# Kernel optimization log

Hardware: AMD Instinct MI355X
Metric: run time of the kernel (lower is better)

The kernel has to match this reference:

```python
import jax, jax.numpy as jnp
import numpy as np

NUM_SITES = 64
BOND_DIM = 64
PHYS_DIM = 2
BATCH = 8192
INIT_STD = 0.125  # 1/sqrt(bond_dim)
EPS_AMP = 1e-12
EPS_LOG = 1e-30


def setup_inputs() -> dict:
    key = jax.random.key(0)
    k_cfg, k_l, k_b, k_r = jax.random.split(key, 4)
    configurations = jax.random.randint(k_cfg, (BATCH, NUM_SITES), 0, PHYS_DIM, dtype=jnp.int32)
    left = jax.random.normal(k_l, (PHYS_DIM, BOND_DIM), dtype=jnp.float32) * INIT_STD
    bulk = jax.random.normal(k_b, (NUM_SITES - 2, BOND_DIM, PHYS_DIM, BOND_DIM), dtype=jnp.float32) * INIT_STD
    right = jax.random.normal(k_r, (BOND_DIM, PHYS_DIM), dtype=jnp.float32) * INIT_STD
    return {"configurations": configurations, "left": left, "bulk": bulk, "right": right}


def _psi(configurations, left, bulk, right):
    # configurations: [B, S] int; left: [d, D]; bulk: [S-2, D, d, D]; right: [D, d]
    B = configurations.shape[0]
    env0 = left[configurations[:, 0]]  # [B, D]
    cfg_mid = configurations[:, 1:-1].T  # [S-2, B]

    def step(env, xs):
        site_t, idx = xs  # site_t: [D, d, D], idx: [B]
        D = site_t.shape[0]
        # env @ site (contract left bond), then gather the per-sample physical slice
        tmp = (env @ site_t.reshape(D, -1)).reshape(B, PHYS_DIM, D)  # [B, d, D]
        env = jnp.take_along_axis(tmp, idx[:, None, None], axis=1)[:, 0, :]  # [B, D]
        return env, None

    env, _ = jax.lax.scan(step, env0, (bulk, cfg_mid))
    cols = jnp.take(right, configurations[:, -1], axis=1).T  # [B, D]
    return jnp.sum(env * cols, axis=1)  # [B]


def _log_norm(left, bulk, right):
    env0 = left.T @ left  # [D, D]  (real dtype -> conj trivial)

    def step(carry, site_t):
        env, log_scale = carry
        sm = jnp.transpose(site_t, (1, 0, 2))  # [d, D, D]
        env = jnp.einsum('pdi,de,pej->ij', sm, env, sm)  # sum_p A_p^H env A_p
        scale = jnp.maximum(jnp.max(jnp.abs(env)), EPS_LOG)
        return (env / scale, log_scale + jnp.log(scale)), None

    (env, log_scale), _ = jax.lax.scan(step, (env0, jnp.zeros((), left.dtype)), bulk)
    z = jnp.sum(right * (env @ right))
    return jnp.log(jnp.maximum(z, EPS_LOG)) + log_scale


def reference(configurations, left, bulk, right):
    psi = _psi(configurations, left, bulk, right)
    abs_sq = jnp.maximum(psi * psi, EPS_AMP)
    log_z = _log_norm(left, bulk, right)
    nll = -(jnp.log(abs_sq) - log_z)
    return jnp.mean(nll)
```

## Files before the change

kernel.cpp:

```cpp
#include <hip/hip_runtime.h>
#include <math.h>

#define NBULK 62
#define SB    72

typedef __attribute__((ext_vector_type(8))) short bf8_t;
typedef __attribute__((ext_vector_type(4))) float f4_t;
typedef __attribute__((ext_vector_type(16))) float f16v_t;

#define MFMA16(a, b, c) __builtin_amdgcn_mfma_f32_16x16x32_bf16((a), (b), (c), 0, 0, 0)
#define MFMA32(a, b, c) __builtin_amdgcn_mfma_f32_32x32x16_bf16((a), (b), (c), 0, 0, 0)

__device__ __forceinline__ unsigned short f2bf(float f) {
    unsigned int u = __float_as_uint(f);
    return (unsigned short)((u + 0x7FFFu + ((u >> 16) & 1u)) >> 16);
}
__device__ __forceinline__ float bf2f(unsigned short h) {
    return __uint_as_float(((unsigned int)h) << 16);
}
__device__ __forceinline__ unsigned cvtpk(float lo, float hi) {
    unsigned r;
    asm("v_cvt_pk_bf16_f32 %0, %1, %2" : "=v"(r) : "v"(lo), "v"(hi));
    return r;
}

__device__ __forceinline__ void gload16(const void* g, void* l) {
    __builtin_amdgcn_global_load_lds(
        (const __attribute__((address_space(1))) unsigned int*)g,
        (__attribute__((address_space(3))) unsigned int*)l, 16, 0, 0);
}

#define WS_E_OFF   1024
#define WS_B_OFF   6144
#define WS_BT_OFF  45056
#define WS_MR_OFF  1060864


extern "C" __global__ __launch_bounds__(256)
void mps_precompute(const float* __restrict__ bulkG,
                    unsigned short* __restrict__ BTg,
                    unsigned short* __restrict__ MRg,
                    float* __restrict__ wsF)
{
    __shared__ unsigned short BTl[8192];
    __shared__ unsigned short MRl[8192];
    const int s = blockIdx.x, tid = threadIdx.x;
    if (s == 0 && tid == 0) {
        wsF[0] = 0.f; wsF[1] = 0.f; wsF[2] = 0.f; wsF[3] = 0.f;
    }
    const float4* src = (const float4*)(bulkG + (size_t)s * 8192);
    for (int c = 0; c < 8; ++c) {
        int idx = tid + c * 256;
        float4 v = src[idx];
        int f  = idx * 4;
        int kk = f >> 7;
        int p  = (f >> 6) & 1;
        int j  = f & 63;
        unsigned short b0 = f2bf(v.x), b1 = f2bf(v.y), b2 = f2bf(v.z), b3 = f2bf(v.w);
        int n = p * 64 + kk;
        int off = n * 64 + (((j >> 3) ^ (n & 7)) << 3) + (j & 7);
        MRl[off + 0] = b0; MRl[off + 1] = b1; MRl[off + 2] = b2; MRl[off + 3] = b3;
        unsigned short bb[4] = {b0, b1, b2, b3};
        #pragma unroll
        for (int t2 = 0; t2 < 4; ++t2) {
            int n2 = p * 64 + j + t2;
            BTl[n2 * 64 + (((kk >> 3) ^ (n2 & 7)) << 3) + (kk & 7)] = bb[t2];
        }
    }
    __syncthreads();
    const uint4* bt4 = (const uint4*)BTl;
    const uint4* mr4 = (const uint4*)MRl;
    uint4* btg = (uint4*)(BTg + (size_t)s * 8192);
    uint4* mrg = (uint4*)(MRg + (size_t)s * 8192);
    for (int c = 0; c < 4; ++c) {
        int idx = tid + c * 256;
        btg[idx] = bt4[idx];
        mrg[idx] = mr4[idx];
    }
}

__device__ __forceinline__ void psi_phase(
    uint4 (&R)[16], int tt, unsigned short* env, const char* BTb,
    const int (&off)[4], unsigned selLo, unsigned selHi,
    int s, int hi, int e7, const f16v_t& Z)
{
    bf8_t benv[4];
    #pragma unroll
    for (int ks = 0; ks < 4; ++ks)
        benv[ks] = *(const bf8_t*)((const char*)env + s * 128 + (((ks * 2 + hi) ^ e7) << 4));
    unsigned sbit = (tt + 1 < 32) ? (selLo >> (tt + 1)) : (selHi >> (tt - 31));
    const bool takeB = (sbit & 1u) != 0u;
    #pragma unroll
    for (int jt = 0; jt < 2; ++jt) {
        f16v_t a0 = Z, a1 = Z;
        #pragma unroll
        for (int ks = 0; ks < 4; ++ks) {
            a0 = MFMA32(*(const bf8_t*)&R[jt * 4 + ks],     benv[ks], a0);
            a1 = MFMA32(*(const bf8_t*)&R[8 + jt * 4 + ks], benv[ks], a1);
        }
        #pragma unroll
        for (int b = 0; b < 4; ++b) {
            float v0 = takeB ? a1[4 * b + 0] : a0[4 * b + 0];
            float v1 = takeB ? a1[4 * b + 1] : a0[4 * b + 1];
            float v2 = takeB ? a1[4 * b + 2] : a0[4 * b + 2];
            float v3 = takeB ? a1[4 * b + 3] : a0[4 * b + 3];
            uint2 w;
            w.x = cvtpk(v0, v1);
            w.y = cvtpk(v2, v3);
            *(uint2*)((char*)env + s * 128 + (((jt * 4 + b) ^ e7) << 4) + hi * 8) = w;
        }
    }
    if (tt + 2 < NBULK) {
        const char* tb = BTb + (size_t)(tt + 2) * 16384;
        #pragma unroll
        for (int p = 0; p < 2; ++p)
            #pragma unroll
            for (int jt = 0; jt < 2; ++jt)
                #pragma unroll
                for (int ks = 0; ks < 4; ++ks)
                    R[p * 8 + jt * 4 + ks] =
                        *(const uint4*)(tb + p * 8192 + jt * 4096 + off[ks]);
    }
}

extern "C" __global__ __launch_bounds__(256)
void mps_main(const int* __restrict__ cfgG, const float* __restrict__ leftG,
              const float* __restrict__ rightG, float* __restrict__ wsF,
              const unsigned short* __restrict__ BTg,
              const unsigned short* __restrict__ MRg)
{
    extern __shared__ char smem[];
    unsigned short* smem16 = (unsigned short*)smem;
    const int tid  = threadIdx.x;
    const int bid  = blockIdx.x;
    const int wv   = tid >> 6;
    const int lane = tid & 63;

    if (bid >= 2) {
        if (wv >= 2) return;
        const int s  = lane & 31;
        const int hi = lane >> 5;
        const int e7 = lane & 7;
        unsigned short* env = smem16 + wv * 2048;
        const int s0 = (bid - 2) * 64 + wv * 32;

        int off[4];
        #pragma unroll
        for (int ks = 0; ks < 4; ++ks)
            off[ks] = s * 128 + (((ks * 2 + hi) ^ e7) << 4);

        const char* BTb = (const char*)BTg;
        uint4 ra[16], rb[16];
        #pragma unroll
        for (int p = 0; p < 2; ++p)
            #pragma unroll
            for (int jt = 0; jt < 2; ++jt)
                #pragma unroll
                for (int ks = 0; ks < 4; ++ks) {
                    ra[p * 8 + jt * 4 + ks] = *(const uint4*)(BTb + p * 8192 + jt * 4096 + off[ks]);
                    rb[p * 8 + jt * 4 + ks] = *(const uint4*)(BTb + 16384 + p * 8192 + jt * 4096 + off[ks]);
                }

        unsigned mbits = 0;
        {
            const int4* crow = (const int4*)(cfgG + (size_t)(s0 + s) * 64 + hi * 32);
            #pragma unroll
            for (int c = 0; c < 8; ++c) {
                int4 v = crow[c];
                mbits |= (unsigned)(v.x & 1) << (c * 4 + 0);
                mbits |= (unsigned)(v.y & 1) << (c * 4 + 1);
                mbits |= (unsigned)(v.z & 1) << (c * 4 + 2);
                mbits |= (unsigned)(v.w & 1) << (c * 4 + 3);
            }
        }
        unsigned other = __shfl_xor(mbits, 32);
        unsigned selLo = hi ? other : mbits;
        unsigned selHi = hi ? mbits : other;

        {
            const float* lp = leftG + (selLo & 1u) * 64 + hi * 32;
            #pragma unroll
            for (int gg = 0; gg < 4; ++gg) {
                float4 a = *(const float4*)(lp + gg * 8);
                float4 b = *(const float4*)(lp + gg * 8 + 4);
                uint4 w;
                w.x = (unsigned)f2bf(a.x) | ((unsigned)f2bf(a.y) << 16);
                w.y = (unsigned)f2bf(a.z) | ((unsigned)f2bf(a.w) << 16);
                w.z = (unsigned)f2bf(b.x) | ((unsigned)f2bf(b.y) << 16);
                w.w = (unsigned)f2bf(b.z) | ((unsigned)f2bf(b.w) << 16);
                int g = hi * 4 + gg;
                *(uint4*)((char*)env + s * 128 + ((g ^ e7) << 4)) = w;
            }
        }

        const f16v_t Z = {0.f};
        for (int t = 0; t < NBULK; t += 2) {
            psi_phase(ra, t,     env, BTb, off, selLo, selHi, s, hi, e7, Z);
            psi_phase(rb, t + 1, env, BTb, off, selLo, selHi, s, hi, e7, Z);
        }

        {
            int selL = (selHi >> 31) & 1;
            float psum = 0.f;
            #pragma unroll
            for (int gg = 0; gg < 4; ++gg) {
                int g = hi * 4 + gg;
                bf8_t e = *(const bf8_t*)((const char*)env + s * 128 + ((g ^ e7) << 4));
                #pragma unroll
                for (int j = 0; j < 8; ++j)
                    psum = fmaf(bf2f((unsigned short)e[j]), rightG[(g * 8 + j) * 2 + selL], psum);
            }
            psum += __shfl_xor(psum, 32);
            float lp = logf(fmaxf(psum * psum, 1e-12f));
            if (hi) lp = 0.f;
            #pragma unroll
            for (int o = 1; o < 64; o <<= 1) lp += __shfl_xor(lp, o);
            if (lane == 0) atomicAdd(&wsF[0], lp);
        }
    } else {
        unsigned short* Ebf = smem16;
        unsigned short* St0 = Ebf + 64 * SB;
        unsigned short* St1 = St0 + 64 * SB;
        unsigned short* Ms0 = St1 + 64 * SB;
        unsigned short* Ms1 = Ms0 + 8192;
        float* wred = (float*)(Ms1 + 8192);

        const int quad = lane >> 4;
        const int ln   = lane & 15;
        const bool fwd = (bid == 0);
        const unsigned short* srcbase = fwd ? BTg : MRg;
        {
            int i = tid >> 2, jq = tid & 3;
            for (int jj = 0; jj < 16; ++jj) {
                int j = jq * 16 + jj;
                float v;
                if (fwd) v = leftG[i] * leftG[j] + leftG[64 + i] * leftG[64 + j];
                else     v = rightG[i * 2] * rightG[j * 2] + rightG[i * 2 + 1] * rightG[j * 2 + 1];
                Ebf[i * SB + j] = f2bf(v);
            }
        }
        {
            int st = fwd ? 0 : 61;
            const char* g = (const char*)(srcbase + (size_t)st * 8192);
            for (int c = 0; c < 4; ++c) {
                int chunk = wv * 4 + c;
                gload16(g + chunk * 1024 + (size_t)lane * 16, (char*)Ms0 + chunk * 1024);
            }
        }
        float lsum = 0.f;
        const int p   = wv >> 1;
        const int ntb = (wv & 1) * 2;
        const int mta = (wv >> 1) * 2;
        const int nta = (wv & 1) * 2;
        unsigned short* Stp = p ? St1 : St0;

        for (int k = 0; k < 31; ++k) {
            __syncthreads();
            unsigned short* M = (k & 1) ? Ms1 : Ms0;
            if (k + 1 < 31) {
                int sn = fwd ? (k + 1) : (61 - (k + 1));
                const char* g = (const char*)(srcbase + (size_t)sn * 8192);
                char* l = (char*)((k & 1) ? Ms0 : Ms1);
                for (int c = 0; c < 4; ++c) {
                    int chunk = wv * 4 + c;
                    gload16(g + chunk * 1024 + (size_t)lane * 16, l + chunk * 1024);
                }
            }
            float inv = 1.f;
            if (k > 0) {
                const float* wp = wred + ((k - 1) & 1) * 4;
                float mm = fmaxf(fmaxf(wp[0], wp[1]), fmaxf(wp[2], wp[3]));
                float sc = fmaxf(mm, 1e-30f);
                inv = 1.f / sc;
                if (tid == 0) lsum += logf(sc);
            }
            {
                bf8_t Af2[4][2];
                #pragma unroll
                for (int mt = 0; mt < 4; ++mt)
                    #pragma unroll
                    for (int h = 0; h < 2; ++h)
                        Af2[mt][h] = *(const bf8_t*)(Ebf + (mt * 16 + ln) * SB + h * 32 + quad * 8);
                #pragma unroll
                for (int c = 0; c < 2; ++c) {
                    int nt = ntb + c;
                    int row = p * 64 + nt * 16 + ln;
                    bf8_t B0 = *(const bf8_t*)(M + row * 64 + (((0 + quad) ^ (ln & 7)) << 3));
                    bf8_t B1 = *(const bf8_t*)(M + row * 64 + (((4 + quad) ^ (ln & 7)) << 3));
                    #pragma unroll
                    for (int mt = 0; mt < 4; ++mt) {
                        f4_t a = {0.f, 0.f, 0.f, 0.f};
                        a = MFMA16(Af2[mt][0], B0, a);
                        a = MFMA16(Af2[mt][1], B1, a);
                        ushort4 pk;
                        pk.x = f2bf(a[0]); pk.y = f2bf(a[1]); pk.z = f2bf(a[2]); pk.w = f2bf(a[3]);
                        *(ushort4*)(Stp + (nt * 16 + ln) * SB + mt * 16 + quad * 4) = pk;
                    }
                }
            }
            asm volatile("s_waitcnt lgkmcnt(0)" ::: "memory");
            __builtin_amdgcn_s_barrier();
            __builtin_amdgcn_sched_barrier(0);
            {
                bf8_t Aw[2][2][2], Bw[2][2][2];
                #pragma unroll
                for (int pp = 0; pp < 2; ++pp)
                    #pragma unroll
                    for (int mi = 0; mi < 2; ++mi)
                        #pragma unroll
                        for (int h = 0; h < 2; ++h)
                            Aw[pp][mi][h] = *(const bf8_t*)(M + (pp * 64 + (mta + mi) * 16 + ln) * 64
                                                              + (((h * 4 + quad) ^ (ln & 7)) << 3));
                #pragma unroll
                for (int pp = 0; pp < 2; ++pp)
                    #pragma unroll
                    for (int ni = 0; ni < 2; ++ni)
                        #pragma unroll
                        for (int h = 0; h < 2; ++h)
                            Bw[pp][ni][h] = *(const bf8_t*)((pp ? St1 : St0)
                                                            + ((nta + ni) * 16 + ln) * SB + h * 32 + quad * 8);
                float mx = 0.f;
                #pragma unroll
                for (int mi = 0; mi < 2; ++mi)
                    #pragma unroll
                    for (int ni = 0; ni < 2; ++ni) {
                        f4_t a = {0.f, 0.f, 0.f, 0.f};
                        #pragma unroll
                        for (int pp = 0; pp < 2; ++pp)
                            #pragma unroll
                            for (int h = 0; h < 2; ++h)
                                a = MFMA16(Aw[pp][mi][h], Bw[pp][ni][h], a);
                        float x0 = a[0] * inv, x1 = a[1] * inv, x2 = a[2] * inv, x3 = a[3] * inv;
                        mx = fmaxf(mx, fmaxf(fmaxf(fabsf(x0), fabsf(x1)), fmaxf(fabsf(x2), fabsf(x3))));
                        ushort4 pk;
                        pk.x = f2bf(x0); pk.y = f2bf(x1); pk.z = f2bf(x2); pk.w = f2bf(x3);
                        *(ushort4*)(Ebf + ((nta + ni) * 16 + ln) * SB + (mta + mi) * 16 + quad * 4) = pk;
                    }
                #pragma unroll
                for (int off2 = 32; off2 > 0; off2 >>= 1)
                    mx = fmaxf(mx, __shfl_xor(mx, off2));
                if (lane == 0) wred[(k & 1) * 4 + wv] = mx;
            }
        }
        __syncthreads();
        float* dst = wsF + (fwd ? WS_E_OFF : WS_B_OFF);
        for (int c = 0; c < 16; ++c) {
            int idx = tid + c * 256;
            dst[idx] = bf2f(Ebf[(idx >> 6) * SB + (idx & 63)]);
        }
        if (tid == 0) wsF[fwd ? 1 : 2] = lsum;
    }
}

extern "C" __global__ void mps_finalize(const float* __restrict__ wsF, float* __restrict__ out)
{
    const int lane = threadIdx.x;
    const float* E  = wsF + WS_E_OFF;
    const float* Bm = wsF + WS_B_OFF;
    float a = 0.f;
    #pragma unroll 8
    for (int j = 0; j < 64; ++j)
        a = fmaf(E[lane * 64 + j], Bm[lane * 64 + j], a);
    #pragma unroll
    for (int off = 32; off > 0; off >>= 1)
        a += __shfl_down(a, off);
    if (lane == 0) {
        const float z = fmaxf(a, 1e-30f);
        const float log_z = logf(z) + wsF[1] + wsF[2];
        out[0] = log_z - wsF[0] * (1.0f / 8192.0f);
    }
}

extern "C" void kernel_launch(void* const* d_in, const int* in_sizes, int n_in,
                              void* d_out, int out_size, void* d_ws, size_t ws_size,
                              hipStream_t stream)
{
    const int*   cfg   = (const int*)d_in[0];
    const float* left  = (const float*)d_in[1];
    const float* bulk  = (const float*)d_in[2];
    const float* right = (const float*)d_in[3];
    float* wsF = (float*)d_ws;
    unsigned short* BTg = (unsigned short*)((char*)d_ws + WS_BT_OFF);
    unsigned short* MRg = (unsigned short*)((char*)d_ws + WS_MR_OFF);

    mps_precompute<<<dim3(62), dim3(256), 0, stream>>>(bulk, BTg, MRg, wsF);
    mps_main<<<dim3(130), dim3(256), 60480, stream>>>(cfg, left, right, wsF, BTg, MRg);
    mps_finalize<<<dim3(1), dim3(64), 0, stream>>>(wsF, (float*)d_out);
}
```

Before: 119.0 us.

## Keep psi env in registers, use all four waves, fuse finalize into main kernel

The psi chain now passes the environment between sites directly in registers, repacking MFMA accumulators into B operands, so the per-site LDS round trip is gone. All four waves per block now run the chain, so the grid shrinks from 130 to 66 blocks. The separate finalize kernel is replaced by a last-block-done atomic counter inside the main kernel, which saves one launch. In exchange it adds fence and atomic overhead, depends on the counter at wsF[3] being zeroed, and may change the register permutation of env elements.

```diff
diff --git a/kernel.cpp b/kernel.cpp
--- a/kernel.cpp
+++ b/kernel.cpp
@@ -79,144 +79,161 @@
     }
 }
 
-__device__ __forceinline__ void psi_phase(
-    uint4 (&R)[16], int tt, unsigned short* env, const char* BTb,
-    const int (&off)[4], unsigned selLo, unsigned selHi,
-    int s, int hi, int e7, const f16v_t& Z)
-{
-    bf8_t benv[4];
+
+__device__ __forceinline__ void psi_fetch(uint4 (&A)[16], const char* tb,
+                                          const unsigned (&voff)[8])
+{
+    #pragma unroll
+    for (int p = 0; p < 2; ++p)
+        #pragma unroll
+        for (int jt = 0; jt < 2; ++jt) {
+            const char* bb = tb + p * 8192 + jt * 4096;
+            #pragma unroll
+            for (int ks = 0; ks < 4; ++ks) {
+                uint2 lo  = *(const uint2*)(bb + voff[2 * ks]);
+                uint2 hi8 = *(const uint2*)(bb + voff[2 * ks + 1]);
+                uint4& F = A[p * 8 + jt * 4 + ks];
+                F.x = lo.x; F.y = lo.y; F.z = hi8.x; F.w = hi8.y;
+            }
+        }
+}
+
+__device__ __forceinline__ void psi_mfma(f16v_t (&c)[2][2], const uint4 (&A)[16],
+                                         const bf8_t (&B)[4], const f16v_t& Z)
+{
+    #pragma unroll
+    for (int p = 0; p < 2; ++p)
+        #pragma unroll
+        for (int jt = 0; jt < 2; ++jt)
+            c[p][jt] = Z;
     #pragma unroll
     for (int ks = 0; ks < 4; ++ks)
-        benv[ks] = *(const bf8_t*)((const char*)env + s * 128 + (((ks * 2 + hi) ^ e7) << 4));
-    unsigned sbit = (tt + 1 < 32) ? (selLo >> (tt + 1)) : (selHi >> (tt - 31));
-    const bool takeB = (sbit & 1u) != 0u;
-    #pragma unroll
-    for (int jt = 0; jt < 2; ++jt) {
-        f16v_t a0 = Z, a1 = Z;
-        #pragma unroll
-        for (int ks = 0; ks < 4; ++ks) {
-            a0 = MFMA32(*(const bf8_t*)&R[jt * 4 + ks],     benv[ks], a0);
-            a1 = MFMA32(*(const bf8_t*)&R[8 + jt * 4 + ks], benv[ks], a1);
-        }
-        #pragma unroll
-        for (int b = 0; b < 4; ++b) {
-            float v0 = takeB ? a1[4 * b + 0] : a0[4 * b + 0];
-            float v1 = takeB ? a1[4 * b + 1] : a0[4 * b + 1];
-            float v2 = takeB ? a1[4 * b + 2] : a0[4 * b + 2];
-            float v3 = takeB ? a1[4 * b + 3] : a0[4 * b + 3];
-            uint2 w;
-            w.x = cvtpk(v0, v1);
-            w.y = cvtpk(v2, v3);
-            *(uint2*)((char*)env + s * 128 + (((jt * 4 + b) ^ e7) << 4) + hi * 8) = w;
-        }
-    }
-    if (tt + 2 < NBULK) {
-        const char* tb = BTb + (size_t)(tt + 2) * 16384;
         #pragma unroll
         for (int p = 0; p < 2; ++p)
             #pragma unroll
             for (int jt = 0; jt < 2; ++jt)
-                #pragma unroll
-                for (int ks = 0; ks < 4; ++ks)
-                    R[p * 8 + jt * 4 + ks] =
-                        *(const uint4*)(tb + p * 8192 + jt * 4096 + off[ks]);
-    }
-}
-
-extern "C" __global__ __launch_bounds__(256)
+                c[p][jt] = MFMA32(*(const bf8_t*)&A[p * 8 + jt * 4 + ks], B[ks], c[p][jt]);
+}
+
+__device__ __forceinline__ void psi_pack(bf8_t (&B)[4], const f16v_t (&c)[2][2], bool takeB)
+{
+    #pragma unroll
+    for (int ks = 0; ks < 4; ++ks) {
+        const int jt = ks >> 1, h8 = (ks & 1) * 8;
+        uint4 w;
+        float x0, x1;
+        x0 = takeB ? c[1][jt][h8 + 0] : c[0][jt][h8 + 0];
+        x1 = takeB ? c[1][jt][h8 + 1] : c[0][jt][h8 + 1];
+        w.x = cvtpk(x0, x1);
+        x0 = takeB ? c[1][jt][h8 + 2] : c[0][jt][h8 + 2];
+        x1 = takeB ? c[1][jt][h8 + 3] : c[0][jt][h8 + 3];
+        w.y = cvtpk(x0, x1);
+        x0 = takeB ? c[1][jt][h8 + 4] : c[0][jt][h8 + 4];
+        x1 = takeB ? c[1][jt][h8 + 5] : c[0][jt][h8 + 5];
+        w.z = cvtpk(x0, x1);
+        x0 = takeB ? c[1][jt][h8 + 6] : c[0][jt][h8 + 6];
+        x1 = takeB ? c[1][jt][h8 + 7] : c[0][jt][h8 + 7];
+        w.w = cvtpk(x0, x1);
+        B[ks] = *(const bf8_t*)&w;
+    }
+}
+
+extern "C" __global__ __launch_bounds__(256, 1)
 void mps_main(const int* __restrict__ cfgG, const float* __restrict__ leftG,
               const float* __restrict__ rightG, float* __restrict__ wsF,
               const unsigned short* __restrict__ BTg,
-              const unsigned short* __restrict__ MRg)
+              const unsigned short* __restrict__ MRg,
+              float* __restrict__ outG)
 {
     extern __shared__ char smem[];
     unsigned short* smem16 = (unsigned short*)smem;
+    __shared__ int lastf;
     const int tid  = threadIdx.x;
     const int bid  = blockIdx.x;
     const int wv   = tid >> 6;
     const int lane = tid & 63;
 
     if (bid >= 2) {
-        if (wv >= 2) return;
         const int s  = lane & 31;
         const int hi = lane >> 5;
-        const int e7 = lane & 7;
-        unsigned short* env = smem16 + wv * 2048;
-        const int s0 = (bid - 2) * 64 + wv * 32;
-
-        int off[4];
+        unsigned voff[8];
         #pragma unroll
-        for (int ks = 0; ks < 4; ++ks)
-            off[ks] = s * 128 + (((ks * 2 + hi) ^ e7) << 4);
-
+        for (int g = 0; g < 8; ++g)
+            voff[g] = (unsigned)(s * 128 + (((g ^ (s & 7)) << 4) + hi * 8));
         const char* BTb = (const char*)BTg;
-        uint4 ra[16], rb[16];
-        #pragma unroll
-        for (int p = 0; p < 2; ++p)
-            #pragma unroll
-            for (int jt = 0; jt < 2; ++jt)
-                #pragma unroll
-                for (int ks = 0; ks < 4; ++ks) {
-                    ra[p * 8 + jt * 4 + ks] = *(const uint4*)(BTb + p * 8192 + jt * 4096 + off[ks]);
-                    rb[p * 8 + jt * 4 + ks] = *(const uint4*)(BTb + 16384 + p * 8192 + jt * 4096 + off[ks]);
-                }
-
+
+        uint4 Aa[16], Ab[16];
+        psi_fetch(Aa, BTb, voff);
+        psi_fetch(Ab, BTb + 16384, voff);
+
+        const int s0 = (bid - 2) * 128 + wv * 32;
         unsigned mbits = 0;
         {
             const int4* crow = (const int4*)(cfgG + (size_t)(s0 + s) * 64 + hi * 32);
             #pragma unroll
-            for (int c = 0; c < 8; ++c) {
-                int4 v = crow[c];
-                mbits |= (unsigned)(v.x & 1) << (c * 4 + 0);
-                mbits |= (unsigned)(v.y & 1) << (c * 4 + 1);
-                mbits |= (unsigned)(v.z & 1) << (c * 4 + 2);
-                mbits |= (unsigned)(v.w & 1) << (c * 4 + 3);
+            for (int c2 = 0; c2 < 8; ++c2) {
+                int4 v = crow[c2];
+                mbits |= (unsigned)(v.x & 1) << (c2 * 4 + 0);
+                mbits |= (unsigned)(v.y & 1) << (c2 * 4 + 1);
+                mbits |= (unsigned)(v.z & 1) << (c2 * 4 + 2);
+                mbits |= (unsigned)(v.w & 1) << (c2 * 4 + 3);
             }
         }
         unsigned other = __shfl_xor(mbits, 32);
         unsigned selLo = hi ? other : mbits;
         unsigned selHi = hi ? mbits : other;
 
+        bf8_t B[4];
         {
-            const float* lp = leftG + (selLo & 1u) * 64 + hi * 32;
-            #pragma unroll
-            for (int gg = 0; gg < 4; ++gg) {
-                float4 a = *(const float4*)(lp + gg * 8);
-                float4 b = *(const float4*)(lp + gg * 8 + 4);
+            const float* lp = leftG + (selLo & 1u) * 64;
+            #pragma unroll
+            for (int ks = 0; ks < 4; ++ks) {
                 uint4 w;
-                w.x = (unsigned)f2bf(a.x) | ((unsigned)f2bf(a.y) << 16);
-                w.y = (unsigned)f2bf(a.z) | ((unsigned)f2bf(a.w) << 16);
-                w.z = (unsigned)f2bf(b.x) | ((unsigned)f2bf(b.y) << 16);
-                w.w = (unsigned)f2bf(b.z) | ((unsigned)f2bf(b.w) << 16);
-                int g = hi * 4 + gg;
-                *(uint4*)((char*)env + s * 128 + ((g ^ e7) << 4)) = w;
+                unsigned wd[4];
+                #pragma unroll
+                for (int d = 0; d < 4; ++d) {
+                    int k0 = 16 * ks + 8 * (d >> 1) + 2 * (d & 1) + 4 * hi;
+                    wd[d] = (unsigned)f2bf(lp[k0]) | ((unsigned)f2bf(lp[k0 + 1]) << 16);
+                }
+                w.x = wd[0]; w.y = wd[1]; w.z = wd[2]; w.w = wd[3];
+                B[ks] = *(const bf8_t*)&w;
             }
         }
 
         const f16v_t Z = {0.f};
-        for (int t = 0; t < NBULK; t += 2) {
-            psi_phase(ra, t,     env, BTb, off, selLo, selHi, s, hi, e7, Z);
-            psi_phase(rb, t + 1, env, BTb, off, selLo, selHi, s, hi, e7, Z);
-        }
-
+        f16v_t c[2][2];
+        #define SELBIT(i) ((bool)((((i) < 32) ? (selLo >> (i)) : (selHi >> ((i) - 32))) & 1u))
+        for (int t = 0; t < 60; t += 2) {
+            psi_mfma(c, Aa, B, Z);
+            psi_fetch(Aa, BTb + (size_t)(t + 2) * 16384, voff);
+            psi_pack(B, c, SELBIT(t + 1));
+            psi_mfma(c, Ab, B, Z);
+            psi_fetch(Ab, BTb + (size_t)(t + 3) * 16384, voff);
+            psi_pack(B, c, SELBIT(t + 2));
+        }
+        psi_mfma(c, Aa, B, Z);
+        psi_pack(B, c, SELBIT(61));
+        psi_mfma(c, Ab, B, Z);
         {
-            int selL = (selHi >> 31) & 1;
+            const bool tb2 = SELBIT(62);
+            const int selL = (int)(selHi >> 31) & 1;
             float psum = 0.f;
             #pragma unroll
-            for (int gg = 0; gg < 4; ++gg) {
-                int g = hi * 4 + gg;
-                bf8_t e = *(const bf8_t*)((const char*)env + s * 128 + ((g ^ e7) << 4));
-                #pragma unroll
-                for (int j = 0; j < 8; ++j)
-                    psum = fmaf(bf2f((unsigned short)e[j]), rightG[(g * 8 + j) * 2 + selL], psum);
-            }
+            for (int jt = 0; jt < 2; ++jt)
+                #pragma unroll
+                for (int q = 0; q < 16; ++q) {
+                    float v = tb2 ? c[1][jt][q] : c[0][jt][q];
+                    int idx = 32 * jt + (q & 3) + 8 * (q >> 2) + 4 * hi;
+                    psum = fmaf(v, rightG[idx * 2 + selL], psum);
+                }
             psum += __shfl_xor(psum, 32);
-            float lp = logf(fmaxf(psum * psum, 1e-12f));
-            if (hi) lp = 0.f;
-            #pragma unroll
-            for (int o = 1; o < 64; o <<= 1) lp += __shfl_xor(lp, o);
-            if (lane == 0) atomicAdd(&wsF[0], lp);
-        }
+            float lp2 = logf(fmaxf(psum * psum, 1e-12f));
+            if (hi) lp2 = 0.f;
+            #pragma unroll
+            for (int o = 1; o < 64; o <<= 1) lp2 += __shfl_xor(lp2, o);
+            if (lane == 0) atomicAdd(&wsF[0], lp2);
+        }
+        #undef SELBIT
     } else {
         unsigned short* Ebf = smem16;
         unsigned short* St0 = Ebf + 64 * SB;
@@ -298,9 +315,7 @@
                     }
                 }
             }
-            asm volatile("s_waitcnt lgkmcnt(0)" ::: "memory");
-            __builtin_amdgcn_s_barrier();
-            __builtin_amdgcn_sched_barrier(0);
+            __syncthreads();
             {
                 bf8_t Aw[2][2][2], Bw[2][2][2];
                 #pragma unroll
@@ -350,24 +365,29 @@
         }
         if (tid == 0) wsF[fwd ? 1 : 2] = lsum;
     }
-}
-
-extern "C" __global__ void mps_finalize(const float* __restrict__ wsF, float* __restrict__ out)
-{
-    const int lane = threadIdx.x;
-    const float* E  = wsF + WS_E_OFF;
-    const float* Bm = wsF + WS_B_OFF;
-    float a = 0.f;
-    #pragma unroll 8
-    for (int j = 0; j < 64; ++j)
-        a = fmaf(E[lane * 64 + j], Bm[lane * 64 + j], a);
-    #pragma unroll
-    for (int off = 32; off > 0; off >>= 1)
-        a += __shfl_down(a, off);
-    if (lane == 0) {
-        const float z = fmaxf(a, 1e-30f);
-        const float log_z = logf(z) + wsF[1] + wsF[2];
-        out[0] = log_z - wsF[0] * (1.0f / 8192.0f);
+
+    __threadfence();
+    if (tid == 0)
+        lastf = (atomicAdd((int*)&wsF[3], 1) == (int)gridDim.x - 1);
+    __syncthreads();
+    if (lastf) {
+        __threadfence();
+        if (wv == 0) {
+            const float* E  = wsF + WS_E_OFF;
+            const float* Bm = wsF + WS_B_OFF;
+            float a = 0.f;
+            #pragma unroll 8
+            for (int c2 = 0; c2 < 64; ++c2)
+                a = fmaf(E[c2 * 64 + lane], Bm[c2 * 64 + lane], a);
+            #pragma unroll
+            for (int o = 32; o > 0; o >>= 1)
+                a += __shfl_down(a, o);
+            if (lane == 0) {
+                const float z = fmaxf(a, 1e-30f);
+                const float log_z = logf(z) + wsF[1] + wsF[2];
+                outG[0] = log_z - wsF[0] * (1.0f / 8192.0f);
+            }
+        }
     }
 }
 
@@ -384,6 +404,6 @@
     unsigned short* MRg = (unsigned short*)((char*)d_ws + WS_MR_OFF);
 
     mps_precompute<<<dim3(62), dim3(256), 0, stream>>>(bulk, BTg, MRg, wsF);
-    mps_main<<<dim3(130), dim3(256), 60480, stream>>>(cfg, left, right, wsF, BTg, MRg);
-    mps_finalize<<<dim3(1), dim3(64), 0, stream>>>(wsF, (float*)d_out);
-}
+    mps_main<<<dim3(66), dim3(256), 60480, stream>>>(cfg, left, right, wsF, BTg, MRg,
+                                                     (float*)d_out);
+}
```

Result: slower. 214.2 us (+80.1%).

## Keep MPS environments in registers using fragment-native weight layout and 16x16 MFMA

Applied to the files above, without the earlier changes.

The precompute pass now stores each bulk site in an MFMA-fragment-native layout, so each lane fetches its operands with contiguous 16-byte loads. The psi chain keeps its environment in registers: the 16x16x32 MFMA output is repacked straight into the next B operand instead of going through shared memory. All four waves are used with 16 samples each rather than two waves with 32. The norm chain computes each wave's column slice using register-held operands and only exchanges results through a small LDS buffer. This removes LDS round-trips and the dynamic shared allocation, at the cost of more register pressure (launch bounds set to one block) and more global weight traffic per wave.

```diff
diff --git a/kernel.cpp b/kernel.cpp
--- a/kernel.cpp
+++ b/kernel.cpp
@@ -1,15 +1,10 @@
 #include <hip/hip_runtime.h>
 #include <math.h>
 
-#define NBULK 62
-#define SB    72
-
 typedef __attribute__((ext_vector_type(8))) short bf8_t;
 typedef __attribute__((ext_vector_type(4))) float f4_t;
-typedef __attribute__((ext_vector_type(16))) float f16v_t;
 
 #define MFMA16(a, b, c) __builtin_amdgcn_mfma_f32_16x16x32_bf16((a), (b), (c), 0, 0, 0)
-#define MFMA32(a, b, c) __builtin_amdgcn_mfma_f32_32x32x16_bf16((a), (b), (c), 0, 0, 0)
 
 __device__ __forceinline__ unsigned short f2bf(float f) {
     unsigned int u = __float_as_uint(f);
@@ -24,26 +19,20 @@
     return r;
 }
 
-__device__ __forceinline__ void gload16(const void* g, void* l) {
-    __builtin_amdgcn_global_load_lds(
-        (const __attribute__((address_space(1))) unsigned int*)g,
-        (__attribute__((address_space(3))) unsigned int*)l, 16, 0, 0);
-}
-
 #define WS_E_OFF   1024
 #define WS_B_OFF   6144
-#define WS_BT_OFF  45056
-#define WS_MR_OFF  1060864
+#define WS_NFF_OFF 45056
+#define WS_NFB_OFF 1060864
 
 
 extern "C" __global__ __launch_bounds__(256)
 void mps_precompute(const float* __restrict__ bulkG,
-                    unsigned short* __restrict__ BTg,
-                    unsigned short* __restrict__ MRg,
+                    unsigned short* __restrict__ NFfG,
+                    unsigned short* __restrict__ NFbG,
                     float* __restrict__ wsF)
 {
-    __shared__ unsigned short BTl[8192];
-    __shared__ unsigned short MRl[8192];
+    __shared__ unsigned short Ff[8192];
+    __shared__ unsigned short Fb[8192];
     const int s = blockIdx.x, tid = threadIdx.x;
     if (s == 0 && tid == 0) {
         wsF[0] = 0.f; wsF[1] = 0.f; wsF[2] = 0.f; wsF[3] = 0.f;
@@ -55,299 +44,293 @@
         int f  = idx * 4;
         int kk = f >> 7;
         int p  = (f >> 6) & 1;
-        int j  = f & 63;
-        unsigned short b0 = f2bf(v.x), b1 = f2bf(v.y), b2 = f2bf(v.z), b3 = f2bf(v.w);
-        int n = p * 64 + kk;
-        int off = n * 64 + (((j >> 3) ^ (n & 7)) << 3) + (j & 7);
-        MRl[off + 0] = b0; MRl[off + 1] = b1; MRl[off + 2] = b2; MRl[off + 3] = b3;
-        unsigned short bb[4] = {b0, b1, b2, b3};
+        int j0 = f & 63;
+        float vals[4] = {v.x, v.y, v.z, v.w};
+        int qf = (kk >> 2) & 3, rf = kk & 3, mf = kk >> 4;
+        int ksf = mf >> 1, jjf = (mf & 1) * 4 + rf;
+        int tb = kk >> 4, lnb = kk & 15;
         #pragma unroll
         for (int t2 = 0; t2 < 4; ++t2) {
-            int n2 = p * 64 + j + t2;
-            BTl[n2 * 64 + (((kk >> 3) ^ (n2 & 7)) << 3) + (kk & 7)] = bb[t2];
+            int j = j0 + t2;
+            unsigned short b = f2bf(vals[t2]);
+            int tf = j >> 4, lnf = j & 15;
+            Ff[((p * 4 + tf) * 2 + ksf) * 512 + (qf * 16 + lnf) * 8 + jjf] = b;
+            int qb = (j >> 2) & 3, rb = j & 3, mb = j >> 4;
+            int ksb = mb >> 1, jjb = (mb & 1) * 4 + rb;
+            Fb[((p * 4 + tb) * 2 + ksb) * 512 + (qb * 16 + lnb) * 8 + jjb] = b;
         }
     }
     __syncthreads();
-    const uint4* bt4 = (const uint4*)BTl;
-    const uint4* mr4 = (const uint4*)MRl;
-    uint4* btg = (uint4*)(BTg + (size_t)s * 8192);
-    uint4* mrg = (uint4*)(MRg + (size_t)s * 8192);
+    const uint4* ff4 = (const uint4*)Ff;
+    const uint4* fb4 = (const uint4*)Fb;
+    uint4* fg = (uint4*)(NFfG + (size_t)s * 8192);
+    uint4* bg = (uint4*)(NFbG + (size_t)s * 8192);
     for (int c = 0; c < 4; ++c) {
         int idx = tid + c * 256;
-        btg[idx] = bt4[idx];
-        mrg[idx] = mr4[idx];
-    }
-}
-
-__device__ __forceinline__ void psi_phase(
-    uint4 (&R)[16], int tt, unsigned short* env, const char* BTb,
-    const int (&off)[4], unsigned selLo, unsigned selHi,
-    int s, int hi, int e7, const f16v_t& Z)
-{
-    bf8_t benv[4];
-    #pragma unroll
-    for (int ks = 0; ks < 4; ++ks)
-        benv[ks] = *(const bf8_t*)((const char*)env + s * 128 + (((ks * 2 + hi) ^ e7) << 4));
-    unsigned sbit = (tt + 1 < 32) ? (selLo >> (tt + 1)) : (selHi >> (tt - 31));
-    const bool takeB = (sbit & 1u) != 0u;
-    #pragma unroll
-    for (int jt = 0; jt < 2; ++jt) {
-        f16v_t a0 = Z, a1 = Z;
-        #pragma unroll
-        for (int ks = 0; ks < 4; ++ks) {
-            a0 = MFMA32(*(const bf8_t*)&R[jt * 4 + ks],     benv[ks], a0);
-            a1 = MFMA32(*(const bf8_t*)&R[8 + jt * 4 + ks], benv[ks], a1);
-        }
-        #pragma unroll
-        for (int b = 0; b < 4; ++b) {
-            float v0 = takeB ? a1[4 * b + 0] : a0[4 * b + 0];
-            float v1 = takeB ? a1[4 * b + 1] : a0[4 * b + 1];
-            float v2 = takeB ? a1[4 * b + 2] : a0[4 * b + 2];
-            float v3 = takeB ? a1[4 * b + 3] : a0[4 * b + 3];
-            uint2 w;
-            w.x = cvtpk(v0, v1);
-            w.y = cvtpk(v2, v3);
-            *(uint2*)((char*)env + s * 128 + (((jt * 4 + b) ^ e7) << 4) + hi * 8) = w;
-        }
-    }
-    if (tt + 2 < NBULK) {
-        const char* tb = BTb + (size_t)(tt + 2) * 16384;
+        fg[idx] = ff4[idx];
+        bg[idx] = fb4[idx];
+    }
+}
+
+__device__ __forceinline__ void pfetch(uint4 (&F)[16], const char* tb, int l16)
+{
+    #pragma unroll
+    for (int i = 0; i < 16; ++i)
+        F[i] = *(const uint4*)(tb + i * 1024 + l16);
+}
+
+__device__ __forceinline__ void pstep(f4_t (&a)[2][4], const uint4 (&F)[16],
+                                      const bf8_t (&B)[2])
+{
+    #pragma unroll
+    for (int p = 0; p < 2; ++p)
+        #pragma unroll
+        for (int mt = 0; mt < 4; ++mt) { f4_t z = {0.f, 0.f, 0.f, 0.f}; a[p][mt] = z; }
+    #pragma unroll
+    for (int ks = 0; ks < 2; ++ks)
         #pragma unroll
         for (int p = 0; p < 2; ++p)
             #pragma unroll
-            for (int jt = 0; jt < 2; ++jt)
-                #pragma unroll
-                for (int ks = 0; ks < 4; ++ks)
-                    R[p * 8 + jt * 4 + ks] =
-                        *(const uint4*)(tb + p * 8192 + jt * 4096 + off[ks]);
-    }
-}
-
-extern "C" __global__ __launch_bounds__(256)
+            for (int mt = 0; mt < 4; ++mt)
+                a[p][mt] = MFMA16(*(const bf8_t*)&F[(p * 4 + mt) * 2 + ks], B[ks], a[p][mt]);
+}
+
+__device__ __forceinline__ void ppack(bf8_t (&B)[2], const f4_t (&a)[2][4], bool takeB)
+{
+    #pragma unroll
+    for (int ks = 0; ks < 2; ++ks) {
+        unsigned w[4];
+        #pragma unroll
+        for (int d = 0; d < 4; ++d) {
+            int mt = 2 * ks + (d >> 1), r = (d & 1) * 2;
+            float x0 = takeB ? a[1][mt][r]     : a[0][mt][r];
+            float x1 = takeB ? a[1][mt][r + 1] : a[0][mt][r + 1];
+            w[d] = cvtpk(x0, x1);
+        }
+        uint4 u = {w[0], w[1], w[2], w[3]};
+        B[ks] = *(const bf8_t*)&u;
+    }
+}
+
+__device__ __forceinline__ void norm_site(
+    int k, bool prefetchNext, int snNext, uint4 (&F)[16], uint4 (&Fn)[16],
+    const char* NF, int l16, bf8_t (&A1)[4][2], f4_t (&acc2)[4], float& lsum,
+    unsigned short (&Xs)[2][4][2][512], float (&wred)[2][4],
+    int wv, int lane, int q, int ln)
+{
+    if (prefetchNext)
+        pfetch(Fn, NF + (size_t)snNext * 16384, l16);
+    float inv = 1.f;
+    if (k > 0) {
+        const float* wp = wred[(k - 1) & 1];
+        float mm = fmaxf(fmaxf(wp[0], wp[1]), fmaxf(wp[2], wp[3]));
+        float sc = fmaxf(mm, 1e-30f);
+        inv = 1.f / sc;
+        lsum += logf(sc);
+    }
+    #pragma unroll
+    for (int mt = 0; mt < 4; ++mt) { f4_t z = {0.f, 0.f, 0.f, 0.f}; acc2[mt] = z; }
+    #pragma unroll
+    for (int p = 0; p < 2; ++p) {
+        f4_t acc1[4];
+        #pragma unroll
+        for (int mt = 0; mt < 4; ++mt) { f4_t z = {0.f, 0.f, 0.f, 0.f}; acc1[mt] = z; }
+        #pragma unroll
+        for (int ks = 0; ks < 2; ++ks)
+            #pragma unroll
+            for (int mt = 0; mt < 4; ++mt)
+                acc1[mt] = MFMA16(A1[mt][ks], *(const bf8_t*)&F[(p * 4 + wv) * 2 + ks], acc1[mt]);
+        bf8_t B2[2];
+        #pragma unroll
+        for (int ks = 0; ks < 2; ++ks) {
+            unsigned w[4];
+            #pragma unroll
+            for (int d = 0; d < 4; ++d) {
+                int mt = 2 * ks + (d >> 1), r = (d & 1) * 2;
+                w[d] = cvtpk(acc1[mt][r], acc1[mt][r + 1]);
+            }
+            uint4 u = {w[0], w[1], w[2], w[3]};
+            B2[ks] = *(const bf8_t*)&u;
+        }
+        #pragma unroll
+        for (int ks = 0; ks < 2; ++ks)
+            #pragma unroll
+            for (int mt = 0; mt < 4; ++mt)
+                acc2[mt] = MFMA16(*(const bf8_t*)&F[(p * 4 + mt) * 2 + ks], B2[ks], acc2[mt]);
+    }
+    float mx = 0.f;
+    #pragma unroll
+    for (int mt = 0; mt < 4; ++mt)
+        #pragma unroll
+        for (int r = 0; r < 4; ++r) {
+            float x = acc2[mt][r] * inv;
+            acc2[mt][r] = x;
+            mx = fmaxf(mx, fabsf(x));
+        }
+    #pragma unroll
+    for (int ks = 0; ks < 2; ++ks) {
+        unsigned w[4];
+        #pragma unroll
+        for (int d = 0; d < 4; ++d) {
+            int mt = 2 * ks + (d >> 1), r = (d & 1) * 2;
+            w[d] = cvtpk(acc2[mt][r], acc2[mt][r + 1]);
+        }
+        uint4 u = {w[0], w[1], w[2], w[3]};
+        *(uint4*)&Xs[(k + 1) & 1][wv][ks][lane * 8] = u;
+    }
+    #pragma unroll
+    for (int o = 32; o > 0; o >>= 1) mx = fmaxf(mx, __shfl_xor(mx, o));
+    if (lane == 0) wred[k & 1][wv] = mx;
+    __syncthreads();
+    if (k < 30) {
+        #pragma unroll
+        for (int mt = 0; mt < 4; ++mt)
+            #pragma unroll
+            for (int ks = 0; ks < 2; ++ks)
+                A1[mt][ks] = *(const bf8_t*)&Xs[(k + 1) & 1][mt][ks][lane * 8];
+    }
+}
+
+extern "C" __global__ __launch_bounds__(256, 1)
 void mps_main(const int* __restrict__ cfgG, const float* __restrict__ leftG,
               const float* __restrict__ rightG, float* __restrict__ wsF,
-              const unsigned short* __restrict__ BTg,
-              const unsigned short* __restrict__ MRg)
-{
-    extern __shared__ char smem[];
-    unsigned short* smem16 = (unsigned short*)smem;
+              const unsigned short* __restrict__ NFfG,
+              const unsigned short* __restrict__ NFbG)
+{
+    __shared__ unsigned short Xs[2][4][2][512];
+    __shared__ float wred[2][4];
     const int tid  = threadIdx.x;
     const int bid  = blockIdx.x;
     const int wv   = tid >> 6;
     const int lane = tid & 63;
+    const int ln   = lane & 15, q = lane >> 4;
+    const int l16  = lane * 16;
 
     if (bid >= 2) {
-        if (wv >= 2) return;
-        const int s  = lane & 31;
-        const int hi = lane >> 5;
-        const int e7 = lane & 7;
-        unsigned short* env = smem16 + wv * 2048;
-        const int s0 = (bid - 2) * 64 + wv * 32;
-
-        int off[4];
-        #pragma unroll
-        for (int ks = 0; ks < 4; ++ks)
-            off[ks] = s * 128 + (((ks * 2 + hi) ^ e7) << 4);
-
-        const char* BTb = (const char*)BTg;
-        uint4 ra[16], rb[16];
-        #pragma unroll
-        for (int p = 0; p < 2; ++p)
-            #pragma unroll
-            for (int jt = 0; jt < 2; ++jt)
+        const char* NF = (const char*)NFfG;
+        uint4 Fa[16], Fb[16];
+        pfetch(Fa, NF, l16);
+        pfetch(Fb, NF + 16384, l16);
+        const int s0 = (bid - 2) * 64 + wv * 16;
+        unsigned part = 0;
+        {
+            const int4* crow = (const int4*)(cfgG + (size_t)(s0 + ln) * 64 + q * 16);
+            #pragma unroll
+            for (int c = 0; c < 4; ++c) {
+                int4 v = crow[c];
+                part |= (unsigned)(v.x & 1) << (c * 4 + 0);
+                part |= (unsigned)(v.y & 1) << (c * 4 + 1);
+                part |= (unsigned)(v.z & 1) << (c * 4 + 2);
+                part |= (unsigned)(v.w & 1) << (c * 4 + 3);
+            }
+        }
+        unsigned pp   = __shfl_xor(part, 16);
+        unsigned comb = (q & 1) ? (pp | (part << 16)) : (part | (pp << 16));
+        unsigned selLo = __shfl(comb, ln);
+        unsigned selHi = __shfl(comb, ln + 32);
+
+        bf8_t B[2];
+        {
+            const float* lp = leftG + (selLo & 1u) * 64;
+            #pragma unroll
+            for (int ks = 0; ks < 2; ++ks) {
+                unsigned w[4];
                 #pragma unroll
-                for (int ks = 0; ks < 4; ++ks) {
-                    ra[p * 8 + jt * 4 + ks] = *(const uint4*)(BTb + p * 8192 + jt * 4096 + off[ks]);
-                    rb[p * 8 + jt * 4 + ks] = *(const uint4*)(BTb + 16384 + p * 8192 + jt * 4096 + off[ks]);
+                for (int d = 0; d < 4; ++d) {
+                    int k0 = 16 * (2 * ks + (d >> 1)) + 4 * q + 2 * (d & 1);
+                    w[d] = (unsigned)f2bf(lp[k0]) | ((unsigned)f2bf(lp[k0 + 1]) << 16);
                 }
-
-        unsigned mbits = 0;
+                uint4 u = {w[0], w[1], w[2], w[3]};
+                B[ks] = *(const bf8_t*)&u;
+            }
+        }
+        f4_t a[2][4];
+        #define SELBIT(i) ((bool)((((i) < 32) ? (selLo >> (i)) : (selHi >> ((i) - 32))) & 1u))
+        for (int t = 0; t < 60; t += 2) {
+            pstep(a, Fa, B);
+            pfetch(Fa, NF + (size_t)(t + 2) * 16384, l16);
+            ppack(B, a, SELBIT(t + 1));
+            pstep(a, Fb, B);
+            pfetch(Fb, NF + (size_t)(t + 3) * 16384, l16);
+            ppack(B, a, SELBIT(t + 2));
+        }
+        pstep(a, Fa, B);
+        ppack(B, a, SELBIT(61));
+        pstep(a, Fb, B);
         {
-            const int4* crow = (const int4*)(cfgG + (size_t)(s0 + s) * 64 + hi * 32);
-            #pragma unroll
-            for (int c = 0; c < 8; ++c) {
-                int4 v = crow[c];
-                mbits |= (unsigned)(v.x & 1) << (c * 4 + 0);
-                mbits |= (unsigned)(v.y & 1) << (c * 4 + 1);
-                mbits |= (unsigned)(v.z & 1) << (c * 4 + 2);
-                mbits |= (unsigned)(v.w & 1) << (c * 4 + 3);
-            }
-        }
-        unsigned other = __shfl_xor(mbits, 32);
-        unsigned selLo = hi ? other : mbits;
-        unsigned selHi = hi ? mbits : other;
-
+            bool tb2 = SELBIT(62);
+            int selL = (int)(selHi >> 31) & 1;
+            float psum = 0.f;
+            #pragma unroll
+            for (int mt = 0; mt < 4; ++mt)
+                #pragma unroll
+                for (int r = 0; r < 4; ++r) {
+                    float v = tb2 ? a[1][mt][r] : a[0][mt][r];
+                    psum = fmaf(v, rightG[(16 * mt + 4 * q + r) * 2 + selL], psum);
+                }
+            psum += __shfl_xor(psum, 16);
+            psum += __shfl_xor(psum, 32);
+            float lp2 = (lane < 16) ? logf(fmaxf(psum * psum, 1e-12f)) : 0.f;
+            #pragma unroll
+            for (int o = 1; o < 64; o <<= 1) lp2 += __shfl_xor(lp2, o);
+            if (lane == 0) atomicAdd(&wsF[0], lp2);
+        }
+        #undef SELBIT
+    } else {
+        const bool fwd = (bid == 0);
+        const char* NF = fwd ? (const char*)NFfG : (const char*)NFbG;
+        uint4 Fa[16], Fb[16];
+        pfetch(Fa, NF + (size_t)(fwd ? 0 : 61) * 16384, l16);
+        bf8_t A1[4][2];
         {
-            const float* lp = leftG + (selLo & 1u) * 64 + hi * 32;
-            #pragma unroll
-            for (int gg = 0; gg < 4; ++gg) {
-                float4 a = *(const float4*)(lp + gg * 8);
-                float4 b = *(const float4*)(lp + gg * 8 + 4);
-                uint4 w;
-                w.x = (unsigned)f2bf(a.x) | ((unsigned)f2bf(a.y) << 16);
-                w.y = (unsigned)f2bf(a.z) | ((unsigned)f2bf(a.w) << 16);
-                w.z = (unsigned)f2bf(b.x) | ((unsigned)f2bf(b.y) << 16);
-                w.w = (unsigned)f2bf(b.z) | ((unsigned)f2bf(b.w) << 16);
-                int g = hi * 4 + gg;
-                *(uint4*)((char*)env + s * 128 + ((g ^ e7) << 4)) = w;
-            }
-        }
-
-        const f16v_t Z = {0.f};
-        for (int t = 0; t < NBULK; t += 2) {
-            psi_phase(ra, t,     env, BTb, off, selLo, selHi, s, hi, e7, Z);
-            psi_phase(rb, t + 1, env, BTb, off, selLo, selHi, s, hi, e7, Z);
-        }
-
-        {
-            int selL = (selHi >> 31) & 1;
-            float psum = 0.f;
-            #pragma unroll
-            for (int gg = 0; gg < 4; ++gg) {
-                int g = hi * 4 + gg;
-                bf8_t e = *(const bf8_t*)((const char*)env + s * 128 + ((g ^ e7) << 4));
+            float li0[4], li1[4];
+            #pragma unroll
+            for (int mt = 0; mt < 4; ++mt) {
+                int m = mt * 16 + ln;
+                li0[mt] = fwd ? leftG[m]      : rightG[m * 2];
+                li1[mt] = fwd ? leftG[64 + m] : rightG[m * 2 + 1];
+            }
+            #pragma unroll
+            for (int ks = 0; ks < 2; ++ks) {
+                float k0v[8], k1v[8];
                 #pragma unroll
-                for (int j = 0; j < 8; ++j)
-                    psum = fmaf(bf2f((unsigned short)e[j]), rightG[(g * 8 + j) * 2 + selL], psum);
-            }
-            psum += __shfl_xor(psum, 32);
-            float lp = logf(fmaxf(psum * psum, 1e-12f));
-            if (hi) lp = 0.f;
-            #pragma unroll
-            for (int o = 1; o < 64; o <<= 1) lp += __shfl_xor(lp, o);
-            if (lane == 0) atomicAdd(&wsF[0], lp);
-        }
-    } else {
-        unsigned short* Ebf = smem16;
-        unsigned short* St0 = Ebf + 64 * SB;
-        unsigned short* St1 = St0 + 64 * SB;
-        unsigned short* Ms0 = St1 + 64 * SB;
-        unsigned short* Ms1 = Ms0 + 8192;
-        float* wred = (float*)(Ms1 + 8192);
-
-        const int quad = lane >> 4;
-        const int ln   = lane & 15;
-        const bool fwd = (bid == 0);
-        const unsigned short* srcbase = fwd ? BTg : MRg;
-        {
-            int i = tid >> 2, jq = tid & 3;
-            for (int jj = 0; jj < 16; ++jj) {
-                int j = jq * 16 + jj;
-                float v;
-                if (fwd) v = leftG[i] * leftG[j] + leftG[64 + i] * leftG[64 + j];
-                else     v = rightG[i * 2] * rightG[j * 2] + rightG[i * 2 + 1] * rightG[j * 2 + 1];
-                Ebf[i * SB + j] = f2bf(v);
-            }
-        }
-        {
-            int st = fwd ? 0 : 61;
-            const char* g = (const char*)(srcbase + (size_t)st * 8192);
-            for (int c = 0; c < 4; ++c) {
-                int chunk = wv * 4 + c;
-                gload16(g + chunk * 1024 + (size_t)lane * 16, (char*)Ms0 + chunk * 1024);
+                for (int jj = 0; jj < 8; ++jj) {
+                    int K = 16 * (2 * ks + (jj >> 2)) + 4 * q + (jj & 3);
+                    k0v[jj] = fwd ? leftG[K]      : rightG[K * 2];
+                    k1v[jj] = fwd ? leftG[64 + K] : rightG[K * 2 + 1];
+                }
+                #pragma unroll
+                for (int mt = 0; mt < 4; ++mt) {
+                    unsigned w[4];
+                    #pragma unroll
+                    for (int d = 0; d < 4; ++d) {
+                        float x0 = li0[mt] * k0v[2 * d]     + li1[mt] * k1v[2 * d];
+                        float x1 = li0[mt] * k0v[2 * d + 1] + li1[mt] * k1v[2 * d + 1];
+                        w[d] = cvtpk(x0, x1);
+                    }
+                    uint4 u = {w[0], w[1], w[2], w[3]};
+                    A1[mt][ks] = *(const bf8_t*)&u;
+                }
             }
         }
         float lsum = 0.f;
-        const int p   = wv >> 1;
-        const int ntb = (wv & 1) * 2;
-        const int mta = (wv >> 1) * 2;
-        const int nta = (wv & 1) * 2;
-        unsigned short* Stp = p ? St1 : St0;
-
-        for (int k = 0; k < 31; ++k) {
-            __syncthreads();
-            unsigned short* M = (k & 1) ? Ms1 : Ms0;
-            if (k + 1 < 31) {
-                int sn = fwd ? (k + 1) : (61 - (k + 1));
-                const char* g = (const char*)(srcbase + (size_t)sn * 8192);
-                char* l = (char*)((k & 1) ? Ms0 : Ms1);
-                for (int c = 0; c < 4; ++c) {
-                    int chunk = wv * 4 + c;
-                    gload16(g + chunk * 1024 + (size_t)lane * 16, l + chunk * 1024);
-                }
-            }
-            float inv = 1.f;
-            if (k > 0) {
-                const float* wp = wred + ((k - 1) & 1) * 4;
-                float mm = fmaxf(fmaxf(wp[0], wp[1]), fmaxf(wp[2], wp[3]));
-                float sc = fmaxf(mm, 1e-30f);
-                inv = 1.f / sc;
-                if (tid == 0) lsum += logf(sc);
-            }
-            {
-                bf8_t Af2[4][2];
-                #pragma unroll
-                for (int mt = 0; mt < 4; ++mt)
-                    #pragma unroll
-                    for (int h = 0; h < 2; ++h)
-                        Af2[mt][h] = *(const bf8_t*)(Ebf + (mt * 16 + ln) * SB + h * 32 + quad * 8);
-                #pragma unroll
-                for (int c = 0; c < 2; ++c) {
-                    int nt = ntb + c;
-                    int row = p * 64 + nt * 16 + ln;
-                    bf8_t B0 = *(const bf8_t*)(M + row * 64 + (((0 + quad) ^ (ln & 7)) << 3));
-                    bf8_t B1 = *(const bf8_t*)(M + row * 64 + (((4 + quad) ^ (ln & 7)) << 3));
-                    #pragma unroll
-                    for (int mt = 0; mt < 4; ++mt) {
-                        f4_t a = {0.f, 0.f, 0.f, 0.f};
-                        a = MFMA16(Af2[mt][0], B0, a);
-                        a = MFMA16(Af2[mt][1], B1, a);
-                        ushort4 pk;
-                        pk.x = f2bf(a[0]); pk.y = f2bf(a[1]); pk.z = f2bf(a[2]); pk.w = f2bf(a[3]);
-                        *(ushort4*)(Stp + (nt * 16 + ln) * SB + mt * 16 + quad * 4) = pk;
-                    }
-                }
-            }
-            asm volatile("s_waitcnt lgkmcnt(0)" ::: "memory");
-            __builtin_amdgcn_s_barrier();
-            __builtin_amdgcn_sched_barrier(0);
-            {
-                bf8_t Aw[2][2][2], Bw[2][2][2];
-                #pragma unroll
-                for (int pp = 0; pp < 2; ++pp)
-                    #pragma unroll
-                    for (int mi = 0; mi < 2; ++mi)
-                        #pragma unroll
-                        for (int h = 0; h < 2; ++h)
-                            Aw[pp][mi][h] = *(const bf8_t*)(M + (pp * 64 + (mta + mi) * 16 + ln) * 64
-                                                              + (((h * 4 + quad) ^ (ln & 7)) << 3));
-                #pragma unroll
-                for (int pp = 0; pp < 2; ++pp)
-                    #pragma unroll
-                    for (int ni = 0; ni < 2; ++ni)
-                        #pragma unroll
-                        for (int h = 0; h < 2; ++h)
-                            Bw[pp][ni][h] = *(const bf8_t*)((pp ? St1 : St0)
-                                                            + ((nta + ni) * 16 + ln) * SB + h * 32 + quad * 8);
-                float mx = 0.f;
-                #pragma unroll
-                for (int mi = 0; mi < 2; ++mi)
-                    #pragma unroll
-                    for (int ni = 0; ni < 2; ++ni) {
-                        f4_t a = {0.f, 0.f, 0.f, 0.f};
-                        #pragma unroll
-                        for (int pp = 0; pp < 2; ++pp)
-                            #pragma unroll
-                            for (int h = 0; h < 2; ++h)
-                                a = MFMA16(Aw[pp][mi][h], Bw[pp][ni][h], a);
-                        float x0 = a[0] * inv, x1 = a[1] * inv, x2 = a[2] * inv, x3 = a[3] * inv;
-                        mx = fmaxf(mx, fmaxf(fmaxf(fabsf(x0), fabsf(x1)), fmaxf(fabsf(x2), fabsf(x3))));
-                        ushort4 pk;
-                        pk.x = f2bf(x0); pk.y = f2bf(x1); pk.z = f2bf(x2); pk.w = f2bf(x3);
-                        *(ushort4*)(Ebf + ((nta + ni) * 16 + ln) * SB + (mta + mi) * 16 + quad * 4) = pk;
-                    }
-                #pragma unroll
-                for (int off2 = 32; off2 > 0; off2 >>= 1)
-                    mx = fmaxf(mx, __shfl_xor(mx, off2));
-                if (lane == 0) wred[(k & 1) * 4 + wv] = mx;
-            }
-        }
-        __syncthreads();
+        f4_t acc2[4];
+        for (int k2 = 0; k2 < 31; k2 += 2) {
+            int sn0 = fwd ? (k2 + 1) : (61 - (k2 + 1));
+            norm_site(k2, k2 + 1 < 31, sn0, Fa, Fb, NF, l16, A1, acc2, lsum,
+                      Xs, wred, wv, lane, q, ln);
+            if (k2 + 1 < 31) {
+                int sn1 = fwd ? (k2 + 2) : (61 - (k2 + 2));
+                norm_site(k2 + 1, k2 + 2 < 31, sn1, Fb, Fa, NF, l16, A1, acc2, lsum,
+                          Xs, wred, wv, lane, q, ln);
+            }
+        }
         float* dst = wsF + (fwd ? WS_E_OFF : WS_B_OFF);
-        for (int c = 0; c < 16; ++c) {
-            int idx = tid + c * 256;
-            dst[idx] = bf2f(Ebf[(idx >> 6) * SB + (idx & 63)]);
-        }
+        #pragma unroll
+        for (int mt = 0; mt < 4; ++mt)
+            #pragma unroll
+            for (int r = 0; r < 4; ++r)
+                dst[(16 * mt + 4 * q + r) * 64 + wv * 16 + ln] = acc2[mt][r];
         if (tid == 0) wsF[fwd ? 1 : 2] = lsum;
     }
 }
@@ -360,7 +343,7 @@
     float a = 0.f;
     #pragma unroll 8
     for (int j = 0; j < 64; ++j)
-        a = fmaf(E[lane * 64 + j], Bm[lane * 64 + j], a);
+        a = fmaf(E[j * 64 + lane], Bm[j * 64 + lane], a);
     #pragma unroll
     for (int off = 32; off > 0; off >>= 1)
         a += __shfl_down(a, off);
@@ -380,10 +363,10 @@
     const float* bulk  = (const float*)d_in[2];
     const float* right = (const float*)d_in[3];
     float* wsF = (float*)d_ws;
-    unsigned short* BTg = (unsigned short*)((char*)d_ws + WS_BT_OFF);
-    unsigned short* MRg = (unsigned short*)((char*)d_ws + WS_MR_OFF);
-
-    mps_precompute<<<dim3(62), dim3(256), 0, stream>>>(bulk, BTg, MRg, wsF);
-    mps_main<<<dim3(130), dim3(256), 60480, stream>>>(cfg, left, right, wsF, BTg, MRg);
+    unsigned short* NFf = (unsigned short*)((char*)d_ws + WS_NFF_OFF);
+    unsigned short* NFb = (unsigned short*)((char*)d_ws + WS_NFB_OFF);
+
+    mps_precompute<<<dim3(62), dim3(256), 0, stream>>>(bulk, NFf, NFb, wsF);
+    mps_main<<<dim3(130), dim3(256), 0, stream>>>(cfg, left, right, wsF, NFf, NFb);
     mps_finalize<<<dim3(1), dim3(64), 0, stream>>>(wsF, (float*)d_out);
 }
```

Result: slower. 219.5 us (+84.6%).
